# Performance work log

Hardware: AMD Instinct MI355X
Metric: run time of the kernel (lower is better)

Reference implementation:

```python
import jax, jax.numpy as jnp
import numpy as np


def setup_inputs() -> dict:
    key = jax.random.key(0)
    k1, k2 = jax.random.split(key)
    B, C, H, W, T = 64, 128, 8, 8, 100
    outputs = jax.random.normal(k1, (B, C, H, W, T), dtype=jnp.float32)
    target = jax.random.uniform(k2, (B, C, H, W, T), dtype=jnp.float32)
    return {"outputs": outputs, "target": target, "n_steps": T, "tau_s": 2}


def _psp(x, tau_s):
    # x: [B, C, H, W, T]; fixed-coefficient leaky integrator over last axis.
    # syn_t = syn_{t-1} * (1 - 1/tau_s) + x_t ; out_t = syn_t / tau_s
    decay = 1.0 - 1.0 / tau_s
    xt = jnp.moveaxis(x, -1, 0)  # [T, B, C, H, W]

    def step(syn, x_t):
        syn = syn * decay + x_t
        return syn, syn / tau_s

    syn0 = jnp.zeros(x.shape[:-1], dtype=x.dtype)
    _, syns = jax.lax.scan(step, syn0, xt)
    return jnp.moveaxis(syns, 0, -1)  # [B, C, H, W, T]


def reference(outputs, target, n_steps, tau_s):
    # n_steps is implied by the trailing axis; kept for signature fidelity.
    target_psp = _psp(target, float(tau_s))
    delta = outputs - target_psp
    return 0.5 * jnp.sum(delta * delta)
```

## Files before the change

### kernel.cpp

```cpp
#include <hip/hip_runtime.h>


constexpr int T  = 100;
constexpr int T4 = T / 4;

__global__ __launch_bounds__(256) void spike_loss_kernel(
    const float4* __restrict__ outs,
    const float4* __restrict__ tgt,
    const int*    __restrict__ tau_p,
    float*        __restrict__ out,
    int n_pixels)
{
    const float tau     = (float)tau_p[0];
    const float inv_tau = 1.0f / tau;
    const float decay   = 1.0f - inv_tau;

    const int pix = blockIdx.x * blockDim.x + threadIdx.x;
    float acc = 0.0f;

    if (pix < n_pixels) {
        const float4* tp = tgt  + (size_t)pix * T4;
        const float4* op = outs + (size_t)pix * T4;
        float syn = 0.0f;
        #pragma unroll 5
        for (int k = 0; k < T4; ++k) {
            const float4 t4 = tp[k];
            const float4 o4 = op[k];
            float d;
            syn = fmaf(syn, decay, t4.x); d = fmaf(-syn, inv_tau, o4.x); acc = fmaf(d, d, acc);
            syn = fmaf(syn, decay, t4.y); d = fmaf(-syn, inv_tau, o4.y); acc = fmaf(d, d, acc);
            syn = fmaf(syn, decay, t4.z); d = fmaf(-syn, inv_tau, o4.z); acc = fmaf(d, d, acc);
            syn = fmaf(syn, decay, t4.w); d = fmaf(-syn, inv_tau, o4.w); acc = fmaf(d, d, acc);
        }
    }

    #pragma unroll
    for (int off = 32; off > 0; off >>= 1)
        acc += __shfl_down(acc, off, 64);

    __shared__ float wave_sums[4];
    const int lane = threadIdx.x & 63;
    const int wid  = threadIdx.x >> 6;
    if (lane == 0) wave_sums[wid] = acc;
    __syncthreads();

    if (threadIdx.x == 0) {
        const float s = wave_sums[0] + wave_sums[1] + wave_sums[2] + wave_sums[3];
        atomicAdd(out, 0.5f * s);
    }
}

extern "C" void kernel_launch(void* const* d_in, const int* in_sizes, int n_in,
                              void* d_out, int out_size, void* d_ws, size_t ws_size,
                              hipStream_t stream) {
    const float* outs = (const float*)d_in[0];
    const float* tgt  = (const float*)d_in[1];
    const int* tau_p  = (const int*)d_in[3];
    float* out        = (float*)d_out;

    const int n_pixels = in_sizes[0] / T;
    const int block = 256;
    const int grid  = (n_pixels + block - 1) / block;

    hipMemsetAsync(out, 0, sizeof(float), stream);

    spike_loss_kernel<<<grid, block, 0, stream>>>(
        (const float4*)outs, (const float4*)tgt, tau_p, out, n_pixels);
}
```

Before: 472.9 us.

## Coalesce loads with lane-parallel scan over time chunks per wave

Instead of one thread walking a whole 100-step pixel with a stride of 400 bytes between threads, each wave now handles two pixels with 25 lanes each. Every lane loads one float4 chunk, so a wave's loads are contiguous and coalesced. The leaky-integrator recurrence becomes a per-chunk partial sum plus a log-step shuffle scan using powers of the decay. A grid-stride loop over a fixed 2048 blocks replaces the per-pixel grid. This leaves 14 of 64 lanes idle, adds shuffle work, and assumes an even pixel count.

```diff
diff --git a/kernel.cpp b/kernel.cpp
--- a/kernel.cpp
+++ b/kernel.cpp
@@ -1,36 +1,66 @@
 #include <hip/hip_runtime.h>
 
 
-constexpr int T  = 100;
-constexpr int T4 = T / 4;
+constexpr int T   = 100;
+constexpr int C4  = 25;
+constexpr int LPW = 50;
 
 __global__ __launch_bounds__(256) void spike_loss_kernel(
-    const float4* __restrict__ outs,
-    const float4* __restrict__ tgt,
+    const float4* __restrict__ tgt4,
+    const float4* __restrict__ outs4,
     const int*    __restrict__ tau_p,
     float*        __restrict__ out,
-    int n_pixels)
+    int n_pairs)
 {
     const float tau     = (float)tau_p[0];
     const float inv_tau = 1.0f / tau;
     const float decay   = 1.0f - inv_tau;
+    const float d2 = decay * decay;
+    const float a1 = d2 * d2;
+    const float a2 = a1 * a1;
+    const float a4 = a2 * a2;
+    const float a8 = a4 * a4;
 
-    const int pix = blockIdx.x * blockDim.x + threadIdx.x;
+    const int lane    = threadIdx.x & 63;
+    const int wave_id = (blockIdx.x * blockDim.x + threadIdx.x) >> 6;
+    const int n_waves = (gridDim.x * blockDim.x) >> 6;
+    const int j       = (lane < C4) ? lane : lane - C4;
+    const bool active = lane < LPW;
+
     float acc = 0.0f;
 
-    if (pix < n_pixels) {
-        const float4* tp = tgt  + (size_t)pix * T4;
-        const float4* op = outs + (size_t)pix * T4;
-        float syn = 0.0f;
-        #pragma unroll 5
-        for (int k = 0; k < T4; ++k) {
-            const float4 t4 = tp[k];
-            const float4 o4 = op[k];
-            float d;
-            syn = fmaf(syn, decay, t4.x); d = fmaf(-syn, inv_tau, o4.x); acc = fmaf(d, d, acc);
-            syn = fmaf(syn, decay, t4.y); d = fmaf(-syn, inv_tau, o4.y); acc = fmaf(d, d, acc);
-            syn = fmaf(syn, decay, t4.z); d = fmaf(-syn, inv_tau, o4.z); acc = fmaf(d, d, acc);
-            syn = fmaf(syn, decay, t4.w); d = fmaf(-syn, inv_tau, o4.w); acc = fmaf(d, d, acc);
+    #pragma unroll 2
+    for (int pp = wave_id; pp < n_pairs; pp += n_waves) {
+        const size_t base = (size_t)pp * LPW + lane;
+        float4 t4, o4;
+        if (active) {
+            t4 = tgt4[base];
+            o4 = outs4[base];
+        } else {
+            t4 = make_float4(0.f, 0.f, 0.f, 0.f);
+            o4 = make_float4(0.f, 0.f, 0.f, 0.f);
+        }
+
+        float s1 = fmaf(t4.x, decay, t4.y);
+        float s2 = fmaf(s1,  decay, t4.z);
+        float s3 = fmaf(s2,  decay, t4.w);
+
+        float X = s3;
+        float y;
+        y = __shfl_up(X, 1, 64); if (j >= 1) X = fmaf(y, a1, X);
+        y = __shfl_up(X, 2, 64); if (j >= 2) X = fmaf(y, a2, X);
+        y = __shfl_up(X, 4, 64); if (j >= 4) X = fmaf(y, a4, X);
+        y = __shfl_up(X, 8, 64); if (j >= 8) X = fmaf(y, a8, X);
+
+        float cin = __shfl_up(X, 1, 64);
+        if (j == 0) cin = 0.0f;
+
+        if (active) {
+            float syn = cin, d;
+            syn = fmaf(syn, decay, t4.x); d = fmaf(syn, -inv_tau, o4.x); acc = fmaf(d, d, acc);
+            syn = fmaf(syn, decay, t4.y); d = fmaf(syn, -inv_tau, o4.y); acc = fmaf(d, d, acc);
+            syn = fmaf(syn, decay, t4.z); d = fmaf(syn, -inv_tau, o4.z); acc = fmaf(d, d, acc);
+            syn = fmaf(syn, decay, t4.w); d = fmaf(syn, -inv_tau, o4.w); acc = fmaf(d, d, acc);
         }
     }
 
@@ -39,8 +69,7 @@
         acc += __shfl_down(acc, off, 64);
 
     __shared__ float wave_sums[4];
-    const int lane = threadIdx.x & 63;
-    const int wid  = threadIdx.x >> 6;
+    const int wid = threadIdx.x >> 6;
     if (lane == 0) wave_sums[wid] = acc;
     __syncthreads();
 
@@ -59,11 +88,13 @@
     float* out        = (float*)d_out;
 
     const int n_pixels = in_sizes[0] / T;
+    const int n_pairs  = n_pixels / 2;
+
     const int block = 256;
-    const int grid  = (n_pixels + block - 1) / block;
+    const int grid  = 2048;
 
     hipMemsetAsync(out, 0, sizeof(float), stream);
 
     spike_loss_kernel<<<grid, block, 0, stream>>>(
-        (const float4*)outs, (const float4*)tgt, tau_p, out, n_pixels);
+        (const float4*)tgt, (const float4*)outs, tau_p, out, n_pairs);
 }
```

New measurement: 415.9 us. 1.14x faster.

## Stage pixel tiles into LDS via async global_load_lds with segmented scan

Applied to the files above, without the earlier changes.

Replaces the one-thread-per-pixel strided float4 loads with a persistent grid of 768 blocks. Each block double-buffers 32-pixel tiles into LDS using the direct global-to-LDS load instruction, so global accesses are fully coalesced. Each pixel's 100-step recurrence is split across 4 threads of 25 steps each, and a shuffle-based carry with precomputed decay powers stitches the segments together, shortening the serial chain. The cost is extra LDS traffic, a block barrier per tile, and an assumption that the pixel count divides evenly by 32.

```diff
diff --git a/kernel.cpp b/kernel.cpp
--- a/kernel.cpp
+++ b/kernel.cpp
@@ -1,53 +1,110 @@
 #include <hip/hip_runtime.h>
 
 
-constexpr int T  = 100;
-constexpr int T4 = T / 4;
+constexpr int T    = 100;
+constexpr int SEG  = 25;
+constexpr int PIX  = 32;
+constexpr int TF   = PIX * T;
+constexpr int FULL = (TF * 4) / 1024;
 
-__global__ __launch_bounds__(256) void spike_loss_kernel(
-    const float4* __restrict__ outs,
-    const float4* __restrict__ tgt,
-    const int*    __restrict__ tau_p,
-    float*        __restrict__ out,
-    int n_pixels)
+typedef const __attribute__((address_space(1))) void* gas_t;
+typedef __attribute__((address_space(3))) void*       las_t;
+
+__global__ __launch_bounds__(128) void spike_loss_kernel(
+    const float* __restrict__ tgt,
+    const float* __restrict__ outs,
+    const int*   __restrict__ tau_p,
+    float*       __restrict__ out,
+    int n_tiles, int tiles_per_block)
 {
+    __shared__ float lds_t[2][TF];
+    __shared__ float lds_o[2][TF];
+    __shared__ float ws[2];
+
     const float tau     = (float)tau_p[0];
     const float inv_tau = 1.0f / tau;
     const float decay   = 1.0f - inv_tau;
+    float d25 = 1.0f;
+    #pragma unroll
+    for (int i = 0; i < SEG; ++i) d25 *= decay;
+    const float d50 = d25 * d25;
 
-    const int pix = blockIdx.x * blockDim.x + threadIdx.x;
+    const int lane = threadIdx.x & 63;
+    const int wv   = threadIdx.x >> 6;
+
+    const int first = blockIdx.x * tiles_per_block;
+    int cnt = n_tiles - first;
+    if (cnt < 0) cnt = 0;
+    if (cnt > tiles_per_block) cnt = tiles_per_block;
+
     float acc = 0.0f;
 
-    if (pix < n_pixels) {
-        const float4* tp = tgt  + (size_t)pix * T4;
-        const float4* op = outs + (size_t)pix * T4;
+    auto stage = [&](int tile, int buf) {
+        const float* gt = tgt  + (size_t)tile * TF;
+        const float* go = outs + (size_t)tile * TF;
+        #pragma unroll
+        for (int i = 0; i < FULL / 2; ++i) {
+            const int c   = i * 2 + wv;
+            const int off = c * 256 + lane * 4;
+            __builtin_amdgcn_global_load_lds((gas_t)(gt + off),
+                (las_t)&lds_t[buf][c * 256], 16, 0, 0);
+            __builtin_amdgcn_global_load_lds((gas_t)(go + off),
+                (las_t)&lds_o[buf][c * 256], 16, 0, 0);
+        }
+        {
+            const int off = FULL * 256 + wv * 64 + lane;
+            __builtin_amdgcn_global_load_lds((gas_t)(gt + off),
+                (las_t)&lds_t[buf][FULL * 256 + wv * 64], 4, 0, 0);
+            __builtin_amdgcn_global_load_lds((gas_t)(go + off),
+                (las_t)&lds_o[buf][FULL * 256 + wv * 64], 4, 0, 0);
+        }
+    };
+
+    auto process = [&](int buf) {
+        const int p    = threadIdx.x >> 2;
+        const int q    = threadIdx.x & 3;
+        const int base = p * T + q * SEG;
+
+        float s[SEG];
         float syn = 0.0f;
-        #pragma unroll 5
-        for (int k = 0; k < T4; ++k) {
-            const float4 t4 = tp[k];
-            const float4 o4 = op[k];
-            float d;
-            syn = fmaf(syn, decay, t4.x); d = fmaf(-syn, inv_tau, o4.x); acc = fmaf(d, d, acc);
-            syn = fmaf(syn, decay, t4.y); d = fmaf(-syn, inv_tau, o4.y); acc = fmaf(d, d, acc);
-            syn = fmaf(syn, decay, t4.z); d = fmaf(-syn, inv_tau, o4.z); acc = fmaf(d, d, acc);
-            syn = fmaf(syn, decay, t4.w); d = fmaf(-syn, inv_tau, o4.w); acc = fmaf(d, d, acc);
+        #pragma unroll
+        for (int i = 0; i < SEG; ++i) {
+            syn = fmaf(syn, decay, lds_t[buf][base + i]);
+            s[i] = syn;
         }
+        const float f1 = __shfl_up(syn, 1, 64);
+        const float f2 = __shfl_up(syn, 2, 64);
+        const float f3 = __shfl_up(syn, 3, 64);
+        float carry = (q >= 1) ? f1 : 0.0f;
+        if (q >= 2) carry = fmaf(f2, d25, carry);
+        if (q >= 3) carry = fmaf(f3, d50, carry);
+
+        float cp = carry;
+        #pragma unroll
+        for (int i = 0; i < SEG; ++i) {
+            cp *= decay;
+            const float st = s[i] + cp;
+            const float d  = fmaf(st, -inv_tau, lds_o[buf][base + i]);
+            acc = fmaf(d, d, acc);
+        }
+    };
+
+    if (cnt > 0) stage(first, 0);
+
+    for (int k = 0; k < cnt; ++k) {
+        asm volatile("s_waitcnt vmcnt(0)" ::: "memory");
+        __syncthreads();
+        if (k + 1 < cnt) stage(first + k + 1, (k + 1) & 1);
+        process(k & 1);
     }
 
     #pragma unroll
     for (int off = 32; off > 0; off >>= 1)
         acc += __shfl_down(acc, off, 64);
-
-    __shared__ float wave_sums[4];
-    const int lane = threadIdx.x & 63;
-    const int wid  = threadIdx.x >> 6;
-    if (lane == 0) wave_sums[wid] = acc;
+    if (lane == 0) ws[wv] = acc;
     __syncthreads();
-
-    if (threadIdx.x == 0) {
-        const float s = wave_sums[0] + wave_sums[1] + wave_sums[2] + wave_sums[3];
-        atomicAdd(out, 0.5f * s);
-    }
+    if (threadIdx.x == 0)
+        atomicAdd(out, 0.5f * (ws[0] + ws[1]));
 }
 
 extern "C" void kernel_launch(void* const* d_in, const int* in_sizes, int n_in,
@@ -59,11 +116,14 @@
     float* out        = (float*)d_out;
 
     const int n_pixels = in_sizes[0] / T;
-    const int block = 256;
-    const int grid  = (n_pixels + block - 1) / block;
+    const int n_tiles  = n_pixels / PIX;
+
+    const int block = 128;
+    const int grid  = 768;
+    const int tiles_per_block = (n_tiles + grid - 1) / grid;
 
     hipMemsetAsync(out, 0, sizeof(float), stream);
 
     spike_loss_kernel<<<grid, block, 0, stream>>>(
-        (const float4*)outs, (const float4*)tgt, tau_p, out, n_pixels);
+        tgt, outs, tau_p, out, n_tiles, tiles_per_block);
 }
```

New measurement: 396.3 us. 1.19x faster.

## Coalesce loads by having each wave process 64 pixels with a segmented shuffle scan

Applied to the files above, without the earlier changes.

Each thread previously walked one pixel's 100-step series, so neighbouring lanes read addresses 400 bytes apart and loads were poorly coalesced. Now a wave reads 64 consecutive float4 chunks per iteration, which is fully contiguous. The leaky-integrator recurrence is recomputed with a segmented parallel prefix scan across lanes using shuffles and decay powers, with a carry passed between iterations. The next chunk is prefetched while the current one is processed. This adds shuffle and ALU work, drops the bounds check so it assumes the pixel count divides evenly, and uses exp2/log2 for the decay powers, which could shift numerics slightly.

```diff
diff --git a/kernel.cpp b/kernel.cpp
--- a/kernel.cpp
+++ b/kernel.cpp
@@ -1,37 +1,80 @@
 #include <hip/hip_runtime.h>
 
 
-constexpr int T  = 100;
-constexpr int T4 = T / 4;
+constexpr int T     = 100;
+constexpr int C4    = 25;
+constexpr int PPW   = 64;
+constexpr int CPW   = C4 * PPW;
+constexpr int ITERS = CPW / 64;
 
-__global__ __launch_bounds__(256) void spike_loss_kernel(
-    const float4* __restrict__ outs,
-    const float4* __restrict__ tgt,
+__global__ __launch_bounds__(256, 8) void spike_loss_kernel(
+    const float4* __restrict__ tgt4,
+    const float4* __restrict__ outs4,
     const int*    __restrict__ tau_p,
-    float*        __restrict__ out,
-    int n_pixels)
+    float*        __restrict__ out)
 {
     const float tau     = (float)tau_p[0];
     const float inv_tau = 1.0f / tau;
-    const float decay   = 1.0f - inv_tau;
+    const float dd1     = 1.0f - inv_tau;
+    const float dd2 = dd1 * dd1;
+    const float dd3 = dd2 * dd1;
+    const float dd4 = dd2 * dd2;
+    const float a1 = dd4;
+    const float a2 = a1 * a1;
+    const float a4 = a2 * a2;
+    const float a8 = a4 * a4;
 
-    const int pix = blockIdx.x * blockDim.x + threadIdx.x;
-    float acc = 0.0f;
+    const int lane    = threadIdx.x & 63;
+    const int wave_id = (blockIdx.x * blockDim.x + threadIdx.x) >> 6;
 
-    if (pix < n_pixels) {
-        const float4* tp = tgt  + (size_t)pix * T4;
-        const float4* op = outs + (size_t)pix * T4;
-        float syn = 0.0f;
-        #pragma unroll 5
-        for (int k = 0; k < T4; ++k) {
-            const float4 t4 = tp[k];
-            const float4 o4 = op[k];
-            float d;
-            syn = fmaf(syn, decay, t4.x); d = fmaf(-syn, inv_tau, o4.x); acc = fmaf(d, d, acc);
-            syn = fmaf(syn, decay, t4.y); d = fmaf(-syn, inv_tau, o4.y); acc = fmaf(d, d, acc);
-            syn = fmaf(syn, decay, t4.z); d = fmaf(-syn, inv_tau, o4.z); acc = fmaf(d, d, acc);
-            syn = fmaf(syn, decay, t4.w); d = fmaf(-syn, inv_tau, o4.w); acc = fmaf(d, d, acc);
-        }
+    const float pw = __builtin_exp2f(4.0f * (float)lane * __builtin_log2f(dd1));
+
+    const float4* tp = tgt4  + (size_t)wave_id * CPW + lane;
+    const float4* op = outs4 + (size_t)wave_id * CPW + lane;
+
+    float acc   = 0.0f;
+    float carry = 0.0f;
+    int   j0    = 0;
+
+    float4 tc = tp[0];
+    float4 oc = op[0];
+
+    for (int it = 0; it < ITERS; ++it) {
+        const int nxt = (it + 1 < ITERS ? it + 1 : it) * 64;
+        const float4 tn = tp[nxt];
+        const float4 on = op[nxt];
+
+        int j = j0 + lane;
+        if (j >= 50) j -= 50;
+        if (j >= 25) j -= 25;
+
+        const float s0 = tc.x;
+        const float s1 = fmaf(s0, dd1, tc.y);
+        const float s2 = fmaf(s1, dd1, tc.z);
+        const float s3 = fmaf(s2, dd1, tc.w);
+
+        float X = s3, y;
+        y = __shfl_up(X, 1, 64); if (j >= 1 && lane >= 1) X = fmaf(y, a1, X);
+        y = __shfl_up(X, 2, 64); if (j >= 2 && lane >= 2) X = fmaf(y, a2, X);
+        y = __shfl_up(X, 4, 64); if (j >= 4 && lane >= 4) X = fmaf(y, a4, X);
+        y = __shfl_up(X, 8, 64); if (j >= 8 && lane >= 8) X = fmaf(y, a8, X);
+
+        const float cinw  = __shfl_up(X, 1, 64);
+        const float cnext = __shfl(X, 63, 64);
+        float cin = (j >= 1 && lane >= 1) ? cinw : 0.0f;
+        if (j0 > 0 && lane < C4 - j0)
+            cin = fmaf(carry, pw, cin);
+
+        float st, d;
+        st = fmaf(cin, dd1, s0); d = fmaf(st, -inv_tau, oc.x); acc = fmaf(d, d, acc);
+        st = fmaf(cin, dd2, s1); d = fmaf(st, -inv_tau, oc.y); acc = fmaf(d, d, acc);
+        st = fmaf(cin, dd3, s2); d = fmaf(st, -inv_tau, oc.z); acc = fmaf(d, d, acc);
+        st = fmaf(cin, dd4, s3); d = fmaf(st, -inv_tau, oc.w); acc = fmaf(d, d, acc);
+
+        carry = cnext;
+        j0 += 64 % C4;
+        if (j0 >= C4) j0 -= C4;
+        tc = tn; oc = on;
     }
 
     #pragma unroll
@@ -39,8 +82,7 @@
         acc += __shfl_down(acc, off, 64);
 
     __shared__ float wave_sums[4];
-    const int lane = threadIdx.x & 63;
-    const int wid  = threadIdx.x >> 6;
+    const int wid = threadIdx.x >> 6;
     if (lane == 0) wave_sums[wid] = acc;
     __syncthreads();
 
@@ -59,11 +101,12 @@
     float* out        = (float*)d_out;
 
     const int n_pixels = in_sizes[0] / T;
-    const int block = 256;
-    const int grid  = (n_pixels + block - 1) / block;
+    const int n_waves  = n_pixels / PPW;
+    const int block    = 256;
+    const int grid     = n_waves * 64 / block;
 
     hipMemsetAsync(out, 0, sizeof(float), stream);
 
     spike_loss_kernel<<<grid, block, 0, stream>>>(
-        (const float4*)outs, (const float4*)tgt, tau_p, out, n_pixels);
+        (const float4*)tgt, (const float4*)outs, tau_p, out);
 }
```

Result: faster. 413.1 us (-12.6%).
